# Optimization experiments

Measured on AMD Instinct MI355X. Metric: run time of the kernel, lower is better.

Reference implementation:

```python
import jax, jax.numpy as jnp
import numpy as np

D_MODEL = 1024
HEAD = 16
HEAD_DIM = D_MODEL // HEAD


def setup_inputs() -> dict:
    key = jax.random.key(0)
    ks = jax.random.split(key, 11)
    B, S = 2, 2048
    q = jax.random.normal(ks[0], (B, S, D_MODEL), dtype=jnp.float32)
    k = jax.random.normal(ks[1], (B, S, D_MODEL), dtype=jnp.float32)
    v = jax.random.normal(ks[2], (B, S, D_MODEL), dtype=jnp.float32)
    # nn.Linear-style params: weight [out, in], bias [out]
    w_scale = 1.0 / np.sqrt(D_MODEL)
    def lin(kk):
        kw, kb = jax.random.split(kk)
        W = jax.random.uniform(kw, (D_MODEL, D_MODEL), jnp.float32, -w_scale, w_scale)
        b = jax.random.uniform(kb, (D_MODEL,), jnp.float32, -w_scale, w_scale)
        return W, b
    Wq, bq = lin(ks[3])
    Wk, bk = lin(ks[4])
    Wv, bv = lin(ks[5])
    Wo, bo = lin(ks[6])
    return {"query": q, "key": k, "value": v,
            "Wq": Wq, "bq": bq, "Wk": Wk, "bk": bk,
            "Wv": Wv, "bv": bv, "Wo": Wo, "bo": bo}


def reference(query, key, value, Wq, bq, Wk, bk, Wv, bv, Wo, bo):
    B, S, _ = query.shape
    # QKV projections (nn.Linear: x @ W.T + b)
    q = query @ Wq.T + bq
    k = key @ Wk.T + bk
    v = value @ Wv.T + bv
    # b s (h d) -> b h s d
    def split_heads(t):
        return t.reshape(B, -1, HEAD, HEAD_DIM).transpose(0, 2, 1, 3)
    q, k, v = split_heads(q), split_heads(k), split_heads(v)
    # NOTE: original forward never applies self.scale, and its masked_fill is
    # non-inplace (result discarded), so scores are raw QK^T with no masking.
    scores = jnp.einsum('bhid,bhjd->bhij', q, k)
    attn = jax.nn.softmax(scores, axis=-1)
    out = jnp.einsum('bhij,bhjd->bhid', attn, v)
    # b h s d -> b s (h d)
    out = out.transpose(0, 2, 1, 3).reshape(B, S, D_MODEL)
    # output projection (dropout=0.0)
    return out @ Wo.T + bo
```

## Files before the change

### kernel.cpp

```cpp
#include <hip/hip_runtime.h>
#include <stdint.h>

#define DM   1024
#define SEQ  2048
#define NH   16
#define HD   64
#define SHIFT 14.0f

typedef _Float16 f16;
typedef f16   half8 __attribute__((ext_vector_type(8)));
typedef f16   half4 __attribute__((ext_vector_type(4)));
typedef float f32x4 __attribute__((ext_vector_type(4)));
typedef float f32x16 __attribute__((ext_vector_type(16)));
typedef unsigned int u32;
typedef u32 u32x4 __attribute__((ext_vector_type(4)));

__device__ __forceinline__ void gl_lds16(const void* g, void* l) {
  __builtin_amdgcn_global_load_lds(
      reinterpret_cast<__attribute__((address_space(1))) u32*>(reinterpret_cast<uintptr_t>(g)),
      reinterpret_cast<__attribute__((address_space(3))) u32*>(reinterpret_cast<uintptr_t>(l)),
      16, 0, 0);
}

__device__ __forceinline__ u32 pkrtz(float a, float b) {
  auto h = __builtin_amdgcn_cvt_pkrtz(a, b);
  return __builtin_bit_cast(u32, h);
}

__global__ __launch_bounds__(256) void cast_all(
    const float* __restrict__ q, const float* __restrict__ k, const float* __restrict__ v,
    const float* __restrict__ Wq, const float* __restrict__ Wk,
    const float* __restrict__ Wv, const float* __restrict__ Wo,
    f16* __restrict__ qh, f16* __restrict__ kh, f16* __restrict__ vh,
    f16* __restrict__ Wqh, f16* __restrict__ Wkh, f16* __restrict__ Wvh,
    f16* __restrict__ Woh) {
  int i = blockIdx.x * 256 + threadIdx.x;
  const float* s;
  f16* d;
  int off;
  float sc = 1.0f;
  if (i < 1572864) {
    int sel = i >> 19;
    off = i & 524287;
    s = sel == 0 ? q : sel == 1 ? k : v;
    d = sel == 0 ? qh : sel == 1 ? kh : vh;
  } else {
    int j = i - 1572864;
    int sel = j >> 17;
    off = j & 131071;
    s = sel == 0 ? Wq : sel == 1 ? Wk : sel == 2 ? Wv : Wo;
    d = sel == 0 ? Wqh : sel == 1 ? Wkh : sel == 2 ? Wvh : Woh;
    if (sel == 0) sc = 1.44269504f;
  }
  const float4* s4 = reinterpret_cast<const float4*>(s);
  float4 a = s4[2 * (size_t)off];
  float4 b = s4[2 * (size_t)off + 1];
  half8 o;
  o[0] = (f16)(sc * a.x); o[1] = (f16)(sc * a.y); o[2] = (f16)(sc * a.z); o[3] = (f16)(sc * a.w);
  o[4] = (f16)(sc * b.x); o[5] = (f16)(sc * b.y); o[6] = (f16)(sc * b.z); o[7] = (f16)(sc * b.w);
  *reinterpret_cast<half8*>(d + 8 * (size_t)off) = o;
}

#define XCD_DECODE                                                             \
  int bid = blockIdx.x;                                                        \
  int xcd = bid & 7;                                                           \
  int idx = bid >> 3;                                               \
  int m0 = (xcd * 4 + (idx >> 3)) * 128;                                       \
  int n0 = (idx & 7) * 128;

__global__ __launch_bounds__(256) void gemm_qkv(
    const f16* __restrict__ A0, const f16* __restrict__ A1, const f16* __restrict__ A2,
    const f16* __restrict__ W0, const f16* __restrict__ W1, const f16* __restrict__ W2,
    const float* __restrict__ b0, const float* __restrict__ b1, const float* __restrict__ b2,
    f16* __restrict__ C0, f16* __restrict__ C1, f16* __restrict__ C2) {
  int z = blockIdx.z;
  const f16* A = (z == 0) ? A0 : (z == 1) ? A1 : A2;
  const f16* W = (z == 0) ? W0 : (z == 1) ? W1 : W2;
  const float* bias = (z == 0) ? b0 : (z == 1) ? b1 : b2;

  XCD_DECODE

  __shared__ f16 As[2][128 * 32];
  __shared__ f16 Ws[2][128 * 32];

  int t = threadIdx.x;
  int w = t >> 6, lane = t & 63, lr = lane & 15, lk = lane >> 4;
  int wr = (w >> 1) * 64, wc = (w & 1) * 64;

  int srow = t >> 2, scol = (t & 3) * 8;
  const f16* ga = A + (size_t)(m0 + srow) * DM + scol;
  const f16* gw = W + (size_t)(n0 + srow) * DM + scol;

  f32x4 zero4 = {0.f, 0.f, 0.f, 0.f};
  f32x4 acc[4][4];
#pragma unroll
  for (int mb = 0; mb < 4; ++mb)
#pragma unroll
    for (int nb = 0; nb < 4; ++nb) acc[mb][nb] = zero4;

  gl_lds16(ga,                    &As[0][t * 8]);
  gl_lds16(ga + (size_t)64 * DM,  &As[0][2048 + t * 8]);
  gl_lds16(gw,                    &Ws[0][t * 8]);
  gl_lds16(gw + (size_t)64 * DM,  &Ws[0][2048 + t * 8]);
  __syncthreads();

  for (int kt = 0; kt < DM / 32; ++kt) {
    int cur = kt & 1;
    if (kt + 1 < DM / 32) {
      int k0 = (kt + 1) * 32;
      gl_lds16(ga + k0,                   &As[cur ^ 1][t * 8]);
      gl_lds16(ga + k0 + (size_t)64 * DM, &As[cur ^ 1][2048 + t * 8]);
      gl_lds16(gw + k0,                   &Ws[cur ^ 1][t * 8]);
      gl_lds16(gw + k0 + (size_t)64 * DM, &Ws[cur ^ 1][2048 + t * 8]);
    }
    half8 af[4], wf[4];
#pragma unroll
    for (int mb = 0; mb < 4; ++mb)
      af[mb] = *reinterpret_cast<const half8*>(&As[cur][(wr + mb * 16 + lr) * 32 + lk * 8]);
#pragma unroll
    for (int nb = 0; nb < 4; ++nb)
      wf[nb] = *reinterpret_cast<const half8*>(&Ws[cur][(wc + nb * 16 + lr) * 32 + lk * 8]);
#pragma unroll
    for (int mb = 0; mb < 4; ++mb)
#pragma unroll
      for (int nb = 0; nb < 4; ++nb)
        acc[mb][nb] = __builtin_amdgcn_mfma_f32_16x16x32_f16(af[mb], wf[nb], acc[mb][nb], 0, 0, 0);
    __syncthreads();
  }

  float bscale = (z == 0) ? 1.44269504f : 1.0f;
  float bv[4];
#pragma unroll
  for (int nb = 0; nb < 4; ++nb) bv[nb] = bias[n0 + wc + nb * 16 + lr] * bscale;

  int lk4 = lk * 4;
  if (z == 2) {
#pragma unroll
    for (int mb = 0; mb < 4; ++mb)
#pragma unroll
      for (int nb = 0; nb < 4; ++nb) {
        int r0 = m0 + wr + mb * 16 + lk4;
        int c = n0 + wc + nb * 16 + lr;
        int b_ = r0 >> 11, s_ = r0 & 2047;
        int h_ = c >> 6, d_ = c & 63;
        f16* dst = C2 + (((size_t)(b_ * NH + h_) * HD + d_) * SEQ + s_);
        half4 hv;
#pragma unroll
        for (int j = 0; j < 4; ++j) hv[j] = (f16)(acc[mb][nb][j] + bv[nb]);
        *reinterpret_cast<half4*>(dst) = hv;
      }
  } else {
    f16* C = (z == 0) ? C0 : C1;
#pragma unroll
    for (int mb = 0; mb < 4; ++mb)
#pragma unroll
      for (int nb = 0; nb < 4; ++nb)
#pragma unroll
        for (int j = 0; j < 4; ++j) {
          int r = m0 + wr + mb * 16 + lk4 + j;
          int c = n0 + wc + nb * 16 + lr;
          C[(size_t)r * DM + c] = (f16)(acc[mb][nb][j] + bv[nb]);
        }
  }
}

__global__ __launch_bounds__(256) void gemm_out(
    const f16* __restrict__ A, const f16* __restrict__ W,
    const float* __restrict__ bias, float* __restrict__ C) {
  XCD_DECODE

  __shared__ f16 As[2][128 * 64];
  __shared__ f16 Ws[2][128 * 64];
  int t = threadIdx.x;
  int w = t >> 6, lane = t & 63, lr = lane & 15, lk = lane >> 4;
  int wr = (w >> 1) * 64, wc = (w & 1) * 64;
  int rloc = 8 * w + (lane >> 3);
  int swc = (lane & 7) ^ (lane >> 3);
  const f16* ga = A + (size_t)(m0 + rloc) * DM + swc * 8;
  const f16* gw = W + (size_t)(n0 + rloc) * DM + swc * 8;
  f32x4 zero4 = {0.f, 0.f, 0.f, 0.f};
  f32x4 acc[4][4];
#pragma unroll
  for (int mb = 0; mb < 4; ++mb)
#pragma unroll
    for (int nb = 0; nb < 4; ++nb) acc[mb][nb] = zero4;
#pragma unroll
  for (int j = 0; j < 4; ++j) {
    gl_lds16(ga + (size_t)(32 * j) * DM, &As[0][j * 2048 + t * 8]);
    gl_lds16(gw + (size_t)(32 * j) * DM, &Ws[0][j * 2048 + t * 8]);
  }
  __syncthreads();
  for (int kt = 0; kt < DM / 64; ++kt) {
    int cur = kt & 1;
    if (kt + 1 < DM / 64) {
      int k0 = (kt + 1) * 64;
#pragma unroll
      for (int j = 0; j < 4; ++j) {
        gl_lds16(ga + (size_t)(32 * j) * DM + k0, &As[cur ^ 1][j * 2048 + t * 8]);
        gl_lds16(gw + (size_t)(32 * j) * DM + k0, &Ws[cur ^ 1][j * 2048 + t * 8]);
      }
    }
#pragma unroll
    for (int ks = 0; ks < 2; ++ks) {
      half8 af[4], wf[4];
#pragma unroll
      for (int mb = 0; mb < 4; ++mb) {
        int R = wr + mb * 16 + lr;
        int c = (ks * 64 + lk * 16) ^ ((lr & 7) << 4);
        af[mb] = *reinterpret_cast<const half8*>(
            reinterpret_cast<const char*>(&As[cur][0]) + R * 128 + c);
      }
#pragma unroll
      for (int nb = 0; nb < 4; ++nb) {
        int R = wc + nb * 16 + lr;
        int c = (ks * 64 + lk * 16) ^ ((lr & 7) << 4);
        wf[nb] = *reinterpret_cast<const half8*>(
            reinterpret_cast<const char*>(&Ws[cur][0]) + R * 128 + c);
      }
#pragma unroll
      for (int mb = 0; mb < 4; ++mb)
#pragma unroll
        for (int nb = 0; nb < 4; ++nb)
          acc[mb][nb] = __builtin_amdgcn_mfma_f32_16x16x32_f16(af[mb], wf[nb], acc[mb][nb], 0, 0, 0);
    }
    __syncthreads();
  }

  float bv[4];
#pragma unroll
  for (int nb = 0; nb < 4; ++nb) bv[nb] = bias[n0 + wc + nb * 16 + lr];
  int lk4 = lk * 4;
#pragma unroll
  for (int mb = 0; mb < 4; ++mb)
#pragma unroll
    for (int nb = 0; nb < 4; ++nb)
#pragma unroll
      for (int j = 0; j < 4; ++j) {
        int r = m0 + wr + mb * 16 + lk4 + j;
        int c = n0 + wc + nb * 16 + lr;
        C[(size_t)r * DM + c] = acc[mb][nb][j] + bv[nb];
      }
}

__global__ __launch_bounds__(256) void attn_fwd15(const f16* __restrict__ Qg,
                                                  const f16* __restrict__ Kg,
                                                  const f16* __restrict__ VTg,
                                                  f16* __restrict__ Og) {
  int bid = blockIdx.x;
  int xcd = bid & 7;
  int slot = bid >> 3;
  int qt = slot & 15;
  int gh = slot >> 4;
  int bh = xcd | (gh << 3);
  int b = bh >> 4, h = bh & 15;

  size_t baseq = (size_t)b * SEQ * DM + (size_t)h * HD;
  const f16* Kp = Kg + baseq;
  const f16* VTp = VTg + (size_t)bh * HD * SEQ;

  __shared__ f16 Kl[2][64 * 128];
  __shared__ f16 Vl[2][64 * 128];

  int t = threadIdx.x;
  int w = t >> 6, lane = t & 63;
  int l31 = lane & 31, lh = lane >> 5;
  int vrow = t >> 4, vcb = t & 15;

  int tt = t >> 4;
  int ku = t & 15;
  int ke = (2 * tt) & 15;
  int kx = ku ^ ke;
  int ksel = (kx >> 3) & 1;
  int kcc = ksel ? ((kx ^ 1) & 7) : kx;
  int kvbase = 2 * tt + ksel;
  const f16* gK = Kp + (size_t)kvbase * DM + kcc * 8;
  const f16* gV = VTp + (size_t)vrow * SEQ + (vcb ^ vrow) * 8;
  f16* lK = &Kl[0][t * 8];
  f16* lV = &Vl[0][vrow * 128 + vcb * 8];
  const int KSTEP = 128 * DM;
  const int VSTEP = 128;
  const int LBK = 64 * 128;
  const int LBV = 64 * 128;

  int qs = qt * 128 + w * 32 + l31;
  const f16* Qrow = Qg + baseq + (size_t)qs * DM;
  half8 qf[4];
#pragma unroll
  for (int s = 0; s < 4; ++s)
    qf[s] = *reinterpret_cast<const half8*>(Qrow + s * 16 + lh * 8);

  auto stage = [&](int kt, int buf) {
    int ko = kt * KSTEP, vo = kt * VSTEP;
#pragma unroll
    for (int j = 0; j < 4; ++j)
      gl_lds16(gK + ko + (size_t)(32 * j) * DM, lK + buf * LBK + j * 2048);
#pragma unroll
    for (int j = 0; j < 4; ++j)
      gl_lds16(gV + vo + (size_t)(16 * j) * SEQ, lV + buf * LBV + j * 16 * 128);
  };
  auto readKf = [&](int buf, int nbk, int s) -> half8 {
    int kv = nbk * 32 + l31;
    int cc = s * 2 + lh;
    int u = (((kv & 1) << 3) | cc) ^ (kv & 15);
    return *reinterpret_cast<const half8*>(
        reinterpret_cast<const char*>(&Kl[buf][0]) + (kv >> 1) * 256 + (u << 4));
  };
  auto readVf = [&](int buf, int mb, int ks) -> half8 {
    int d = mb * 32 + l31;
    int c = (ks * 32 + lh * 16) ^ ((d & 15) << 4);
    return *reinterpret_cast<const half8*>(
        reinterpret_cast<const char*>(&Vl[buf][0]) + d * 256 + c);
  };

  f32x16 mShift, o0, o1;
#pragma unroll
  for (int i = 0; i < 16; ++i) {
    mShift[i] = -SHIFT;
    o0[i] = 0.f;
    o1[i] = 0.f;
  }
  float l_r = 0.f;

  stage(0, 0);
  __syncthreads();

  const int NT = SEQ / 128;
  for (int kt = 0; kt < NT; ++kt) {
    int cur = kt & 1;
    if (kt + 1 < NT) stage(kt + 1, cur ^ 1);

    __builtin_amdgcn_s_setprio(1);
    half8 k0 = readKf(cur, 0, 0);
    half8 k1 = readKf(cur, 1, 0);
    half8 k2 = readKf(cur, 2, 0);
    half8 k3 = readKf(cur, 3, 0);
    f32x16 s0 = __builtin_amdgcn_mfma_f32_32x32x16_f16(k0, qf[0], mShift, 0, 0, 0);
    f32x16 s1 = __builtin_amdgcn_mfma_f32_32x32x16_f16(k1, qf[0], mShift, 0, 0, 0);
    f32x16 s2 = __builtin_amdgcn_mfma_f32_32x32x16_f16(k2, qf[0], mShift, 0, 0, 0);
    f32x16 s3 = __builtin_amdgcn_mfma_f32_32x32x16_f16(k3, qf[0], mShift, 0, 0, 0);
#pragma unroll
    for (int s = 1; s < 4; ++s) {
      k0 = readKf(cur, 0, s);
      k1 = readKf(cur, 1, s);
      k2 = readKf(cur, 2, s);
      k3 = readKf(cur, 3, s);
      s0 = __builtin_amdgcn_mfma_f32_32x32x16_f16(k0, qf[s], s0, 0, 0, 0);
      s1 = __builtin_amdgcn_mfma_f32_32x32x16_f16(k1, qf[s], s1, 0, 0, 0);
      s2 = __builtin_amdgcn_mfma_f32_32x32x16_f16(k2, qf[s], s2, 0, 0, 0);
      s3 = __builtin_amdgcn_mfma_f32_32x32x16_f16(k3, qf[s], s3, 0, 0, 0);
    }
    __builtin_amdgcn_s_setprio(0);

    float rs0 = 0.f, rs1 = 0.f, rs2 = 0.f, rs3 = 0.f;
#pragma unroll
    for (int i = 0; i < 16; ++i) { s0[i] = __builtin_amdgcn_exp2f(s0[i]); rs0 += s0[i]; }
#pragma unroll
    for (int i = 0; i < 16; ++i) { s1[i] = __builtin_amdgcn_exp2f(s1[i]); rs1 += s1[i]; }
#pragma unroll
    for (int i = 0; i < 16; ++i) { s2[i] = __builtin_amdgcn_exp2f(s2[i]); rs2 += s2[i]; }
#pragma unroll
    for (int i = 0; i < 16; ++i) { s3[i] = __builtin_amdgcn_exp2f(s3[i]); rs3 += s3[i]; }
    l_r += (rs0 + rs1) + (rs2 + rs3);

#define PVSTEP(SP, NBK)                                                        \
    {                                                                          \
      u32 u0 = pkrtz(SP[0], SP[1]);                                            \
      u32 u1 = pkrtz(SP[2], SP[3]);                                            \
      u32 u2 = pkrtz(SP[4], SP[5]);                                            \
      u32 u3 = pkrtz(SP[6], SP[7]);                                            \
      u32 u4 = pkrtz(SP[8], SP[9]);                                            \
      u32 u5 = pkrtz(SP[10], SP[11]);                                          \
      u32 u6 = pkrtz(SP[12], SP[13]);                                          \
      u32 u7 = pkrtz(SP[14], SP[15]);                                          \
      asm volatile("v_permlane32_swap_b32 %0, %1" : "+v"(u0), "+v"(u2));       \
      asm volatile("v_permlane32_swap_b32 %0, %1" : "+v"(u1), "+v"(u3));       \
      asm volatile("v_permlane32_swap_b32 %0, %1" : "+v"(u4), "+v"(u6));       \
      asm volatile("v_permlane32_swap_b32 %0, %1" : "+v"(u5), "+v"(u7));       \
      u32x4 w0 = {u0, u1, u2, u3};                                             \
      u32x4 w1 = {u4, u5, u6, u7};                                             \
      half8 pa0 = __builtin_bit_cast(half8, w0);                               \
      half8 pa1 = __builtin_bit_cast(half8, w1);                               \
      half8 va = readVf(cur, 0, 2 * NBK);                                      \
      half8 vb = readVf(cur, 1, 2 * NBK);                                      \
      __builtin_amdgcn_s_setprio(1);                                           \
      o0 = __builtin_amdgcn_mfma_f32_32x32x16_f16(va, pa0, o0, 0, 0, 0);       \
      o1 = __builtin_amdgcn_mfma_f32_32x32x16_f16(vb, pa0, o1, 0, 0, 0);       \
      __builtin_amdgcn_s_setprio(0);                                           \
      va = readVf(cur, 0, 2 * NBK + 1);                                        \
      vb = readVf(cur, 1, 2 * NBK + 1);                                        \
      __builtin_amdgcn_s_setprio(1);                                           \
      o0 = __builtin_amdgcn_mfma_f32_32x32x16_f16(va, pa1, o0, 0, 0, 0);       \
      o1 = __builtin_amdgcn_mfma_f32_32x32x16_f16(vb, pa1, o1, 0, 0, 0);       \
      __builtin_amdgcn_s_setprio(0);                                           \
    }
    PVSTEP(s0, 0)
    PVSTEP(s1, 1)
    PVSTEP(s2, 2)
    PVSTEP(s3, 3)
#undef PVSTEP

    __syncthreads();
  }

  float l_all = l_r + __shfl_xor(l_r, 32);
  float inv = 1.0f / l_all;
  f16* Orow = Og + baseq + (size_t)qs * DM;
#pragma unroll
  for (int mb = 0; mb < 2; ++mb) {
    const f32x16& oo = mb ? o1 : o0;
#pragma unroll
    for (int rq = 0; rq < 4; ++rq) {
      half4 hv;
      hv[0] = (f16)(oo[4 * rq + 0] * inv);
      hv[1] = (f16)(oo[4 * rq + 1] * inv);
      hv[2] = (f16)(oo[4 * rq + 2] * inv);
      hv[3] = (f16)(oo[4 * rq + 3] * inv);
      *reinterpret_cast<half4*>(Orow + mb * 32 + 8 * rq + 4 * lh) = hv;
    }
  }
}

extern "C" void kernel_launch(void* const* d_in, const int* in_sizes, int n_in,
                              void* d_out, int out_size, void* d_ws, size_t ws_size,
                              hipStream_t stream) {
  (void)in_sizes; (void)n_in; (void)out_size; (void)ws_size;
  const float* q  = (const float*)d_in[0];
  const float* k  = (const float*)d_in[1];
  const float* v  = (const float*)d_in[2];
  const float* Wq = (const float*)d_in[3];
  const float* bq = (const float*)d_in[4];
  const float* Wk = (const float*)d_in[5];
  const float* bk = (const float*)d_in[6];
  const float* Wv = (const float*)d_in[7];
  const float* bv = (const float*)d_in[8];
  const float* Wo = (const float*)d_in[9];
  const float* bo = (const float*)d_in[10];
  float* out = (float*)d_out;

  char* ws = (char*)d_ws;
  const size_t MB = 1u << 20;
  f16* qh  = (f16*)(ws + 0 * MB);
  f16* kh  = (f16*)(ws + 8 * MB);
  f16* vh  = (f16*)(ws + 16 * MB);
  f16* Wqh = (f16*)(ws + 24 * MB);
  f16* Wkh = (f16*)(ws + 26 * MB);
  f16* Wvh = (f16*)(ws + 28 * MB);
  f16* Woh = (f16*)(ws + 30 * MB);
  f16* Qp  = (f16*)(ws + 32 * MB);
  f16* Kp  = (f16*)(ws + 40 * MB);
  f16* Vtp = (f16*)(ws + 48 * MB);
  f16* At  = (f16*)(ws + 56 * MB);

  cast_all<<<8192, 256, 0, stream>>>(q, k, v, Wq, Wk, Wv, Wo,
                                     qh, kh, vh, Wqh, Wkh, Wvh, Woh);
  gemm_qkv<<<dim3(256, 1, 3), 256, 0, stream>>>(qh, kh, vh, Wqh, Wkh, Wvh,
                                                bq, bk, bv, Qp, Kp, Vtp);
  attn_fwd15<<<512, 256, 0, stream>>>(Qp, Kp, Vtp, At);
  gemm_out<<<256, 256, 0, stream>>>(At, Woh, bo, out);
}
```

Before: 120.6 us.

## Retile QKV/out GEMMs to 128x64 and double attention query tile per block

gemm_qkv moves to 128x64 output tiles with 512 threads, a K-step of 64 and an XOR-swizzled LDS layout, doubling the grid. gemm_out shrinks its N tile to 64 so it launches twice as many blocks. Attention blocks grow to 512 threads covering 256 query rows, with the first 256 threads staging K/V, so each K/V tile in LDS serves twice as many queries. The aim is better CU occupancy in the GEMMs and less K/V reload traffic in attention. The cost is lower per-wave MFMA reuse in the GEMMs and possible register pressure or spills under the 512-thread launch bound.

```diff
diff --git a/kernel.cpp b/kernel.cpp
--- a/kernel.cpp
+++ b/kernel.cpp
@@ -61,14 +61,14 @@
   *reinterpret_cast<half8*>(d + 8 * (size_t)off) = o;
 }
 
-#define XCD_DECODE                                                             \
+#define XCD_DECODE_N64                                                         \
   int bid = blockIdx.x;                                                        \
   int xcd = bid & 7;                                                           \
   int idx = bid >> 3;                                               \
-  int m0 = (xcd * 4 + (idx >> 3)) * 128;                                       \
-  int n0 = (idx & 7) * 128;
-
-__global__ __launch_bounds__(256) void gemm_qkv(
+  int m0 = (xcd * 4 + (idx >> 4)) * 128;                                       \
+  int n0 = (idx & 15) * 64;
+
+__global__ __launch_bounds__(512) void gemm_qkv(
     const f16* __restrict__ A0, const f16* __restrict__ A1, const f16* __restrict__ A2,
     const f16* __restrict__ W0, const f16* __restrict__ W1, const f16* __restrict__ W2,
     const float* __restrict__ b0, const float* __restrict__ b1, const float* __restrict__ b2,
@@ -78,67 +78,77 @@
   const f16* W = (z == 0) ? W0 : (z == 1) ? W1 : W2;
   const float* bias = (z == 0) ? b0 : (z == 1) ? b1 : b2;
 
-  XCD_DECODE
-
-  __shared__ f16 As[2][128 * 32];
-  __shared__ f16 Ws[2][128 * 32];
+  XCD_DECODE_N64
+
+  __shared__ f16 As[2][128 * 64];
+  __shared__ f16 Ws[2][64 * 64];
 
   int t = threadIdx.x;
   int w = t >> 6, lane = t & 63, lr = lane & 15, lk = lane >> 4;
-  int wr = (w >> 1) * 64, wc = (w & 1) * 64;
-
-  int srow = t >> 2, scol = (t & 3) * 8;
-  const f16* ga = A + (size_t)(m0 + srow) * DM + scol;
-  const f16* gw = W + (size_t)(n0 + srow) * DM + scol;
+  int wr = (w >> 1) * 32;
+  int wc = (w & 1) * 32;
+  int srow = t >> 3;
+  int swc = (t & 7) ^ (srow & 7);
+  const f16* ga = A + (size_t)(m0 + srow) * DM + swc * 8;
+  const f16* gw = W + (size_t)(n0 + srow) * DM + swc * 8;
 
   f32x4 zero4 = {0.f, 0.f, 0.f, 0.f};
-  f32x4 acc[4][4];
-#pragma unroll
-  for (int mb = 0; mb < 4; ++mb)
-#pragma unroll
-    for (int nb = 0; nb < 4; ++nb) acc[mb][nb] = zero4;
+  f32x4 acc[2][2];
+#pragma unroll
+  for (int mb = 0; mb < 2; ++mb)
+#pragma unroll
+    for (int nb = 0; nb < 2; ++nb) acc[mb][nb] = zero4;
 
   gl_lds16(ga,                    &As[0][t * 8]);
-  gl_lds16(ga + (size_t)64 * DM,  &As[0][2048 + t * 8]);
+  gl_lds16(ga + (size_t)64 * DM,  &As[0][4096 + t * 8]);
   gl_lds16(gw,                    &Ws[0][t * 8]);
-  gl_lds16(gw + (size_t)64 * DM,  &Ws[0][2048 + t * 8]);
   __syncthreads();
 
-  for (int kt = 0; kt < DM / 32; ++kt) {
+  for (int kt = 0; kt < DM / 64; ++kt) {
     int cur = kt & 1;
-    if (kt + 1 < DM / 32) {
-      int k0 = (kt + 1) * 32;
+    if (kt + 1 < DM / 64) {
+      int k0 = (kt + 1) * 64;
       gl_lds16(ga + k0,                   &As[cur ^ 1][t * 8]);
-      gl_lds16(ga + k0 + (size_t)64 * DM, &As[cur ^ 1][2048 + t * 8]);
+      gl_lds16(ga + k0 + (size_t)64 * DM, &As[cur ^ 1][4096 + t * 8]);
       gl_lds16(gw + k0,                   &Ws[cur ^ 1][t * 8]);
-      gl_lds16(gw + k0 + (size_t)64 * DM, &Ws[cur ^ 1][2048 + t * 8]);
-    }
-    half8 af[4], wf[4];
-#pragma unroll
-    for (int mb = 0; mb < 4; ++mb)
-      af[mb] = *reinterpret_cast<const half8*>(&As[cur][(wr + mb * 16 + lr) * 32 + lk * 8]);
-#pragma unroll
-    for (int nb = 0; nb < 4; ++nb)
-      wf[nb] = *reinterpret_cast<const half8*>(&Ws[cur][(wc + nb * 16 + lr) * 32 + lk * 8]);
-#pragma unroll
-    for (int mb = 0; mb < 4; ++mb)
-#pragma unroll
-      for (int nb = 0; nb < 4; ++nb)
-        acc[mb][nb] = __builtin_amdgcn_mfma_f32_16x16x32_f16(af[mb], wf[nb], acc[mb][nb], 0, 0, 0);
+    }
+#pragma unroll
+    for (int ks = 0; ks < 2; ++ks) {
+      half8 af[2], wf[2];
+#pragma unroll
+      for (int mb = 0; mb < 2; ++mb) {
+        int R = wr + mb * 16 + lr;
+        int c = (ks * 64 + lk * 16) ^ ((lr & 7) << 4);
+        af[mb] = *reinterpret_cast<const half8*>(
+            reinterpret_cast<const char*>(&As[cur][0]) + R * 128 + c);
+      }
+#pragma unroll
+      for (int nb = 0; nb < 2; ++nb) {
+        int R = wc + nb * 16 + lr;
+        int c = (ks * 64 + lk * 16) ^ ((lr & 7) << 4);
+        wf[nb] = *reinterpret_cast<const half8*>(
+            reinterpret_cast<const char*>(&Ws[cur][0]) + R * 128 + c);
+      }
+#pragma unroll
+      for (int mb = 0; mb < 2; ++mb)
+#pragma unroll
+        for (int nb = 0; nb < 2; ++nb)
+          acc[mb][nb] = __builtin_amdgcn_mfma_f32_16x16x32_f16(af[mb], wf[nb], acc[mb][nb], 0, 0, 0);
+    }
     __syncthreads();
   }
 
   float bscale = (z == 0) ? 1.44269504f : 1.0f;
-  float bv[4];
-#pragma unroll
-  for (int nb = 0; nb < 4; ++nb) bv[nb] = bias[n0 + wc + nb * 16 + lr] * bscale;
+  float bv[2];
+#pragma unroll
+  for (int nb = 0; nb < 2; ++nb) bv[nb] = bias[n0 + wc + nb * 16 + lr] * bscale;
 
   int lk4 = lk * 4;
   if (z == 2) {
 #pragma unroll
-    for (int mb = 0; mb < 4; ++mb)
-#pragma unroll
-      for (int nb = 0; nb < 4; ++nb) {
+    for (int mb = 0; mb < 2; ++mb)
+#pragma unroll
+      for (int nb = 0; nb < 2; ++nb) {
         int r0 = m0 + wr + mb * 16 + lk4;
         int c = n0 + wc + nb * 16 + lr;
         int b_ = r0 >> 11, s_ = r0 & 2047;
@@ -152,9 +162,9 @@
   } else {
     f16* C = (z == 0) ? C0 : C1;
 #pragma unroll
-    for (int mb = 0; mb < 4; ++mb)
-#pragma unroll
-      for (int nb = 0; nb < 4; ++nb)
+    for (int mb = 0; mb < 2; ++mb)
+#pragma unroll
+      for (int nb = 0; nb < 2; ++nb)
 #pragma unroll
         for (int j = 0; j < 4; ++j) {
           int r = m0 + wr + mb * 16 + lk4 + j;
@@ -167,42 +177,46 @@
 __global__ __launch_bounds__(256) void gemm_out(
     const f16* __restrict__ A, const f16* __restrict__ W,
     const float* __restrict__ bias, float* __restrict__ C) {
-  XCD_DECODE
+  XCD_DECODE_N64
 
   __shared__ f16 As[2][128 * 64];
-  __shared__ f16 Ws[2][128 * 64];
+  __shared__ f16 Ws[2][64 * 64];
   int t = threadIdx.x;
   int w = t >> 6, lane = t & 63, lr = lane & 15, lk = lane >> 4;
-  int wr = (w >> 1) * 64, wc = (w & 1) * 64;
+  int wr = (w >> 1) * 64, wc = (w & 1) * 32;
   int rloc = 8 * w + (lane >> 3);
   int swc = (lane & 7) ^ (lane >> 3);
   const f16* ga = A + (size_t)(m0 + rloc) * DM + swc * 8;
   const f16* gw = W + (size_t)(n0 + rloc) * DM + swc * 8;
   f32x4 zero4 = {0.f, 0.f, 0.f, 0.f};
-  f32x4 acc[4][4];
+  f32x4 acc[4][2];
 #pragma unroll
   for (int mb = 0; mb < 4; ++mb)
 #pragma unroll
-    for (int nb = 0; nb < 4; ++nb) acc[mb][nb] = zero4;
-#pragma unroll
-  for (int j = 0; j < 4; ++j) {
+    for (int nb = 0; nb < 2; ++nb) acc[mb][nb] = zero4;
+
+#pragma unroll
+  for (int j = 0; j < 4; ++j)
     gl_lds16(ga + (size_t)(32 * j) * DM, &As[0][j * 2048 + t * 8]);
+#pragma unroll
+  for (int j = 0; j < 2; ++j)
     gl_lds16(gw + (size_t)(32 * j) * DM, &Ws[0][j * 2048 + t * 8]);
-  }
   __syncthreads();
+
   for (int kt = 0; kt < DM / 64; ++kt) {
     int cur = kt & 1;
     if (kt + 1 < DM / 64) {
       int k0 = (kt + 1) * 64;
 #pragma unroll
-      for (int j = 0; j < 4; ++j) {
+      for (int j = 0; j < 4; ++j)
         gl_lds16(ga + (size_t)(32 * j) * DM + k0, &As[cur ^ 1][j * 2048 + t * 8]);
+#pragma unroll
+      for (int j = 0; j < 2; ++j)
         gl_lds16(gw + (size_t)(32 * j) * DM + k0, &Ws[cur ^ 1][j * 2048 + t * 8]);
-      }
     }
 #pragma unroll
     for (int ks = 0; ks < 2; ++ks) {
-      half8 af[4], wf[4];
+      half8 af[4], wf[2];
 #pragma unroll
       for (int mb = 0; mb < 4; ++mb) {
         int R = wr + mb * 16 + lr;
@@ -211,7 +225,7 @@
             reinterpret_cast<const char*>(&As[cur][0]) + R * 128 + c);
       }
 #pragma unroll
-      for (int nb = 0; nb < 4; ++nb) {
+      for (int nb = 0; nb < 2; ++nb) {
         int R = wc + nb * 16 + lr;
         int c = (ks * 64 + lk * 16) ^ ((lr & 7) << 4);
         wf[nb] = *reinterpret_cast<const half8*>(
@@ -220,20 +234,20 @@
 #pragma unroll
       for (int mb = 0; mb < 4; ++mb)
 #pragma unroll
-        for (int nb = 0; nb < 4; ++nb)
+        for (int nb = 0; nb < 2; ++nb)
           acc[mb][nb] = __builtin_amdgcn_mfma_f32_16x16x32_f16(af[mb], wf[nb], acc[mb][nb], 0, 0, 0);
     }
     __syncthreads();
   }
 
-  float bv[4];
-#pragma unroll
-  for (int nb = 0; nb < 4; ++nb) bv[nb] = bias[n0 + wc + nb * 16 + lr];
+  float bv[2];
+#pragma unroll
+  for (int nb = 0; nb < 2; ++nb) bv[nb] = bias[n0 + wc + nb * 16 + lr];
   int lk4 = lk * 4;
 #pragma unroll
   for (int mb = 0; mb < 4; ++mb)
 #pragma unroll
-    for (int nb = 0; nb < 4; ++nb)
+    for (int nb = 0; nb < 2; ++nb)
 #pragma unroll
       for (int j = 0; j < 4; ++j) {
         int r = m0 + wr + mb * 16 + lk4 + j;
@@ -242,15 +256,15 @@
       }
 }
 
-__global__ __launch_bounds__(256) void attn_fwd15(const f16* __restrict__ Qg,
+__global__ __launch_bounds__(512) void attn_fwd17(const f16* __restrict__ Qg,
                                                   const f16* __restrict__ Kg,
                                                   const f16* __restrict__ VTg,
                                                   f16* __restrict__ Og) {
   int bid = blockIdx.x;
   int xcd = bid & 7;
   int slot = bid >> 3;
-  int qt = slot & 15;
-  int gh = slot >> 4;
+  int qt = slot & 7;
+  int gh = slot >> 3;
   int bh = xcd | (gh << 3);
   int b = bh >> 4, h = bh & 15;
 
@@ -274,15 +288,15 @@
   int kcc = ksel ? ((kx ^ 1) & 7) : kx;
   int kvbase = 2 * tt + ksel;
   const f16* gK = Kp + (size_t)kvbase * DM + kcc * 8;
-  const f16* gV = VTp + (size_t)vrow * SEQ + (vcb ^ vrow) * 8;
+  const f16* gV = VTp + (size_t)vrow * SEQ + ((vcb ^ vrow) & 15) * 8;
   f16* lK = &Kl[0][t * 8];
-  f16* lV = &Vl[0][vrow * 128 + vcb * 8];
+  f16* lV = &Vl[0][t * 8];
   const int KSTEP = 128 * DM;
   const int VSTEP = 128;
   const int LBK = 64 * 128;
   const int LBV = 64 * 128;
 
-  int qs = qt * 128 + w * 32 + l31;
+  int qs = qt * 256 + w * 32 + l31;
   const f16* Qrow = Qg + baseq + (size_t)qs * DM;
   half8 qf[4];
 #pragma unroll
@@ -290,13 +304,15 @@
     qf[s] = *reinterpret_cast<const half8*>(Qrow + s * 16 + lh * 8);
 
   auto stage = [&](int kt, int buf) {
-    int ko = kt * KSTEP, vo = kt * VSTEP;
-#pragma unroll
-    for (int j = 0; j < 4; ++j)
-      gl_lds16(gK + ko + (size_t)(32 * j) * DM, lK + buf * LBK + j * 2048);
-#pragma unroll
-    for (int j = 0; j < 4; ++j)
-      gl_lds16(gV + vo + (size_t)(16 * j) * SEQ, lV + buf * LBV + j * 16 * 128);
+    if (t < 256) {
+      int ko = kt * KSTEP, vo = kt * VSTEP;
+#pragma unroll
+      for (int j = 0; j < 4; ++j)
+        gl_lds16(gK + ko + (size_t)(32 * j) * DM, lK + buf * LBK + j * 2048);
+#pragma unroll
+      for (int j = 0; j < 4; ++j)
+        gl_lds16(gV + vo + (size_t)(16 * j) * SEQ, lV + buf * LBV + j * 2048);
+    }
   };
   auto readKf = [&](int buf, int nbk, int s) -> half8 {
     int kv = nbk * 32 + l31;
@@ -453,8 +469,8 @@
 
   cast_all<<<8192, 256, 0, stream>>>(q, k, v, Wq, Wk, Wv, Wo,
                                      qh, kh, vh, Wqh, Wkh, Wvh, Woh);
-  gemm_qkv<<<dim3(256, 1, 3), 256, 0, stream>>>(qh, kh, vh, Wqh, Wkh, Wvh,
+  gemm_qkv<<<dim3(512, 1, 3), 512, 0, stream>>>(qh, kh, vh, Wqh, Wkh, Wvh,
                                                 bq, bk, bv, Qp, Kp, Vtp);
-  attn_fwd15<<<512, 256, 0, stream>>>(Qp, Kp, Vtp, At);
-  gemm_out<<<256, 256, 0, stream>>>(At, Woh, bo, out);
-}
+  attn_fwd17<<<256, 512, 0, stream>>>(Qp, Kp, Vtp, At);
+  gemm_out<<<512, 256, 0, stream>>>(At, Woh, bo, out);
+}
```

Result: faster. 106.7 us (-11.6%).
